# Optimization experiments

Measured on AMD Instinct MI355X. Metric: run time of the kernel, lower is better.

Reference implementation:

```python
import jax, jax.numpy as jnp
import numpy as np

B, M, FIN, K, FOUT, NNZ = 8, 40000, 64, 6, 64, 320000

def setup_inputs() -> dict:
    key = jax.random.key(0)
    k1, k2, k3, k4, k5 = jax.random.split(key, 5)
    x = jax.random.normal(k1, (B, M, FIN), dtype=jnp.float32)
    edge_rows = jax.random.randint(k2, (NNZ,), 0, M)
    edge_cols = jax.random.randint(k3, (NNZ,), 0, M)
    edge_vals = jax.random.normal(k4, (NNZ,), dtype=jnp.float32) * 0.1
    W = jax.random.normal(k5, (FIN * K, FOUT), dtype=jnp.float32) * 0.05
    return {"x": x, "edge_vals": edge_vals, "W": W,
            "edge_rows": edge_rows, "edge_cols": edge_cols}

def reference(x, edge_vals, W, edge_rows, edge_cols):
    Bd, Md, Fin = x.shape
    nK = W.shape[0] // Fin
    Fout = W.shape[1]
    # x0: [M, Fin*B] as in tf.transpose([1,2,0]) + reshape
    x0 = jnp.transpose(x, (1, 2, 0)).reshape(Md, Fin * Bd)

    def spmm_rescaled(v):
        # rescale_L(L, lmax=2) = L - I, so (L - I) @ v = L@v - v
        Lv = jax.ops.segment_sum(edge_vals[:, None] * v[edge_cols],
                                 edge_rows, num_segments=Md)
        return Lv - v

    xs = [x0]
    if nK > 1:
        x1 = spmm_rescaled(x0)
        xs.append(x1)
        xp, xc = x0, x1
        for _ in range(2, nK):
            xn = 2.0 * spmm_rescaled(xc) - xp  # Chebyshev recurrence
            xs.append(xn)
            xp, xc = xc, xn
    X = jnp.stack(xs, axis=0)                     # [K, M, Fin*B]
    X = X.reshape(nK, Md, Fin, Bd)                # split Fin*B -> (Fin, B)
    X = jnp.transpose(X, (3, 1, 2, 0))            # [B, M, Fin, K]
    X = X.reshape(Bd * Md, Fin * nK)
    out = (X @ W).reshape(Bd, Md, Fout)           # dense projection
    return out
```

## Files before the change

kernel.cpp:

```cpp
#include <hip/hip_runtime.h>

#define Mn    40000
#define Bn    8
#define FINn  64
#define Kn    6
#define FOUTn 64
#define NNZn  320000
#define Cn    512
#define NB    ((Mn + 255) / 256)
#define MT    (Mn / 64)


typedef _Float16 half8 __attribute__((ext_vector_type(8)));
typedef __attribute__((ext_vector_type(4))) float floatx4;

__device__ __forceinline__ ushort f2h(float f) {
    _Float16 h = (_Float16)f;
    return *(ushort*)&h;
}

__device__ __forceinline__ void gl_lds16(const ushort* g, ushort* l) {
    __builtin_amdgcn_global_load_lds(
        (const __attribute__((address_space(1))) unsigned int*)g,
        (__attribute__((address_space(3))) unsigned int*)l, 16, 0, 0);
}


__global__ __launch_bounds__(256) void k_hist(const int* __restrict__ rows,
                                              int* __restrict__ cnt) {
    int e = blockIdx.x * 256 + threadIdx.x;
    if (e < NNZn) atomicAdd(&cnt[rows[e]], 1);
}

__global__ __launch_bounds__(256) void k_scan_part(const int* __restrict__ cnt,
                                                   int* __restrict__ rowptr,
                                                   int* __restrict__ bsum) {
    __shared__ int part[256];
    int tid = threadIdx.x;
    int r = blockIdx.x * 256 + tid;
    int v = (r < Mn) ? cnt[r] : 0;
    part[tid] = v;
    __syncthreads();
    for (int off = 1; off < 256; off <<= 1) {
        int t = (tid >= off) ? part[tid - off] : 0;
        __syncthreads();
        part[tid] += t;
        __syncthreads();
    }
    if (r < Mn) rowptr[r] = part[tid] - v;
    if (tid == 255) bsum[blockIdx.x] = part[255];
}

__global__ __launch_bounds__(256) void k_scan_bsums(const int* __restrict__ bsum,
                                                    int* __restrict__ boff,
                                                    int* __restrict__ rowptr) {
    __shared__ int part[256];
    int tid = threadIdx.x;
    int v = (tid < NB) ? bsum[tid] : 0;
    part[tid] = v;
    __syncthreads();
    for (int off = 1; off < 256; off <<= 1) {
        int t = (tid >= off) ? part[tid - off] : 0;
        __syncthreads();
        part[tid] += t;
        __syncthreads();
    }
    if (tid < NB) boff[tid] = part[tid] - v;
    if (tid == 255) rowptr[Mn] = part[255];
}

__global__ __launch_bounds__(256) void k_scan_add(int* __restrict__ rowptr,
                                                  const int* __restrict__ boff,
                                                  int* __restrict__ wcur) {
    int r = blockIdx.x * 256 + threadIdx.x;
    if (r < Mn) {
        int v = rowptr[r] + boff[blockIdx.x];
        rowptr[r] = v;
        wcur[r] = v;
    }
}

__global__ __launch_bounds__(256) void k_scatter(const int* __restrict__ rows,
                                                 const int* __restrict__ cols,
                                                 const float* __restrict__ vals,
                                                 int* __restrict__ wcur,
                                                 int2* __restrict__ csr) {
    int e = blockIdx.x * 256 + threadIdx.x;
    if (e < NNZn) {
        int p = atomicAdd(&wcur[rows[e]], 1);
        int2 cv; cv.x = cols[e]; cv.y = __float_as_int(vals[e]);
        csr[p] = cv;
    }
}


__global__ __launch_bounds__(256) void k_transpose_h(const float* __restrict__ x,
                                                     ushort* __restrict__ x0h) {
    int m0 = blockIdx.x * 4;
    int t  = threadIdx.x;
#pragma unroll
    for (int k = 0; k < 2; ++k) {
        int i   = t + k * 256;
        int ml  = i >> 7;
        int rem = i & 127;
        int b   = rem >> 4;
        int fq  = (rem & 15) * 4;
        float4 a = *(const float4*)(x + ((size_t)b * Mn + m0 + ml) * 64 + fq);
        union { uint2 u; ushort h[4]; } s;
        s.h[0] = f2h(a.x); s.h[1] = f2h(a.y); s.h[2] = f2h(a.z); s.h[3] = f2h(a.w);
        *(uint2*)(x0h + (size_t)(m0 + ml) * Cn + b * 64 + fq) = s.u;
    }
}


__device__ __forceinline__ void fmah8(float* a, uint4 g, float w) {
    union { uint4 u; _Float16 h[8]; } c; c.u = g;
#pragma unroll
    for (int i = 0; i < 8; ++i) a[i] += w * (float)c.h[i];
}

__global__ __launch_bounds__(256) void k_spmm_h(const ushort* __restrict__ xc,
                                                const ushort* __restrict__ xp,
                                                ushort* __restrict__ xn,
                                                const int* __restrict__ rowptr,
                                                const int2* __restrict__ csr,
                                                int first) {
    int t = threadIdx.x;
    int lane = t & 63;
    int m = blockIdx.x * 4 + (t >> 6);
    const uint4* xc4 = (const uint4*)xc;
    uint4 v = xc4[(size_t)m * 64 + lane];
    uint4 p;
    if (!first) p = ((const uint4*)xp)[(size_t)m * 64 + lane];
    float a[8];
    { union { uint4 u; _Float16 h[8]; } c; c.u = v;
#pragma unroll
      for (int i = 0; i < 8; ++i) a[i] = -(float)c.h[i]; }

    int e = rowptr[m], end = rowptr[m + 1];
    for (; e + 8 <= end; e += 8) {
        int2 cv[8];
#pragma unroll
        for (int i = 0; i < 8; ++i) cv[i] = csr[e + i];
        uint4 g[8];
#pragma unroll
        for (int i = 0; i < 8; ++i) g[i] = xc4[(size_t)cv[i].x * 64 + lane];
#pragma unroll
        for (int i = 0; i < 8; ++i) fmah8(a, g[i], __int_as_float(cv[i].y));
    }
    for (; e + 4 <= end; e += 4) {
        int2 cv0 = csr[e],     cv1 = csr[e + 1];
        int2 cv2 = csr[e + 2], cv3 = csr[e + 3];
        uint4 g0 = xc4[(size_t)cv0.x * 64 + lane];
        uint4 g1 = xc4[(size_t)cv1.x * 64 + lane];
        uint4 g2 = xc4[(size_t)cv2.x * 64 + lane];
        uint4 g3 = xc4[(size_t)cv3.x * 64 + lane];
        fmah8(a, g0, __int_as_float(cv0.y));
        fmah8(a, g1, __int_as_float(cv1.y));
        fmah8(a, g2, __int_as_float(cv2.y));
        fmah8(a, g3, __int_as_float(cv3.y));
    }
    for (; e < end; ++e) {
        int2 cv = csr[e];
        uint4 g = xc4[(size_t)cv.x * 64 + lane];
        fmah8(a, g, __int_as_float(cv.y));
    }

    if (!first) {
        union { uint4 u; _Float16 h[8]; } c; c.u = p;
#pragma unroll
        for (int i = 0; i < 8; ++i) a[i] = 2.f * a[i] - (float)c.h[i];
    }
    union { uint4 u; _Float16 h[8]; } s;
#pragma unroll
    for (int i = 0; i < 8; ++i) s.h[i] = (_Float16)a[i];
    ((uint4*)xn)[(size_t)m * 64 + lane] = s.u;
}


__global__ __launch_bounds__(256) void k_wfrag(const float* __restrict__ W,
                                               ushort* __restrict__ wfrag) {
    int idx = blockIdx.x * 256 + threadIdx.x;
    if (idx >= 12 * 4 * 64 * 8) return;
    int j    = idx & 7;
    int lane = (idx >> 3) & 63;
    int n    = (idx >> 9) & 3;
    int kk   = idx >> 11;
    int k    = (lane >> 4) * 8 + j;
    int lev  = kk >> 1;
    int f    = (kk & 1) * 32 + k;
    int fo   = n * 16 + (lane & 15);
    wfrag[idx] = f2h(W[(f * Kn + lev) * FOUTn + fo]);
}


__global__ __launch_bounds__(256, 4) void k_gemm_mfma(const ushort* __restrict__ xh,
                                                      const ushort* __restrict__ wfrag,
                                                      float* __restrict__ out) {
    __shared__ __align__(16) ushort As[2][4096];
    int t     = threadIdx.x;
    int wv    = t >> 6;
    int lane  = t & 63;
    int q     = lane >> 4, r = lane & 15;
    int mtile = blockIdx.x % MT;
    int b     = blockIdx.x / MT;
    int m0    = mtile * 64;
    int swz   = r & 7;

    const size_t lstrideH = (size_t)Mn * Cn;

    const ushort* wfb = wfrag + ((size_t)wv * 64 + lane) * 8;
    half8 wf0  = *(const half8*)(wfb);
    half8 wf1  = *(const half8*)(wfb + 1 * 2048);
    half8 wf2  = *(const half8*)(wfb + 2 * 2048);
    half8 wf3  = *(const half8*)(wfb + 3 * 2048);
    half8 wf4  = *(const half8*)(wfb + 4 * 2048);
    half8 wf5  = *(const half8*)(wfb + 5 * 2048);
    half8 wf6  = *(const half8*)(wfb + 6 * 2048);
    half8 wf7  = *(const half8*)(wfb + 7 * 2048);
    half8 wf8  = *(const half8*)(wfb + 8 * 2048);
    half8 wf9  = *(const half8*)(wfb + 9 * 2048);
    half8 wf10 = *(const half8*)(wfb + 10 * 2048);
    half8 wf11 = *(const half8*)(wfb + 11 * 2048);

    int srow = wv * 8 + (lane >> 3);
    int gsw  = (lane & 7) ^ (srow & 7);
    const ushort* gsA = xh + (size_t)(m0 + srow) * Cn + b * 64 + gsw * 8;
    const ushort* gsB = gsA + 32 * (size_t)Cn;

    floatx4 acc0 = (floatx4)0.f, acc1 = (floatx4)0.f;
    floatx4 acc2 = (floatx4)0.f, acc3 = (floatx4)0.f;

#define STAGE(lev, buf) do {                                          \
        gl_lds16(gsA + (size_t)(lev) * lstrideH, &As[buf][wv * 512]); \
        gl_lds16(gsB + (size_t)(lev) * lstrideH, &As[buf][2048 + wv * 512]); \
    } while (0)

#define AF(buf, sub, half) \
    (*(const half8*)&As[buf][((sub) * 16 + r) * 64 + (((((half) * 4) + q) ^ swz) << 3)])

#define LEVEL(lev, buf, VMSTR, WFA, WFB) do {                                         \
        asm volatile("s_waitcnt vmcnt(" VMSTR ")" ::: "memory");                      \
        __syncthreads();                                                              \
        half8 a00 = AF(buf, 0, 0); half8 a10 = AF(buf, 1, 0);                         \
        half8 a20 = AF(buf, 2, 0); half8 a30 = AF(buf, 3, 0);                         \
        half8 a01 = AF(buf, 0, 1); half8 a11 = AF(buf, 1, 1);                         \
        half8 a21 = AF(buf, 2, 1); half8 a31 = AF(buf, 3, 1);                         \
        acc0 = __builtin_amdgcn_mfma_f32_16x16x32_f16(a00, WFA, acc0, 0, 0, 0);       \
        acc1 = __builtin_amdgcn_mfma_f32_16x16x32_f16(a10, WFA, acc1, 0, 0, 0);       \
        acc2 = __builtin_amdgcn_mfma_f32_16x16x32_f16(a20, WFA, acc2, 0, 0, 0);       \
        acc3 = __builtin_amdgcn_mfma_f32_16x16x32_f16(a30, WFA, acc3, 0, 0, 0);       \
        acc0 = __builtin_amdgcn_mfma_f32_16x16x32_f16(a01, WFB, acc0, 0, 0, 0);       \
        acc1 = __builtin_amdgcn_mfma_f32_16x16x32_f16(a11, WFB, acc1, 0, 0, 0);       \
        acc2 = __builtin_amdgcn_mfma_f32_16x16x32_f16(a21, WFB, acc2, 0, 0, 0);       \
        acc3 = __builtin_amdgcn_mfma_f32_16x16x32_f16(a31, WFB, acc3, 0, 0, 0);       \
        __syncthreads();                                                              \
        if ((lev) < 4) STAGE((lev) + 2, buf);                                         \
    } while (0)

    STAGE(0, 0);
    STAGE(1, 1);
    LEVEL(0, 0, "2", wf0,  wf1);
    LEVEL(1, 1, "2", wf2,  wf3);
    LEVEL(2, 0, "2", wf4,  wf5);
    LEVEL(3, 1, "2", wf6,  wf7);
    LEVEL(4, 0, "2", wf8,  wf9);
    LEVEL(5, 1, "0", wf10, wf11);

#undef LEVEL
#undef AF
#undef STAGE

#pragma unroll
    for (int sub = 0; sub < 4; ++sub) {
        floatx4 av = (sub == 0) ? acc0 : (sub == 1) ? acc1 : (sub == 2) ? acc2 : acc3;
#pragma unroll
        for (int reg = 0; reg < 4; ++reg) {
            size_t o = ((size_t)b * Mn + m0 + sub * 16 + q * 4 + reg) * FOUTn
                     + wv * 16 + r;
            out[o] = av[reg];
        }
    }
}


__global__ __launch_bounds__(512) void k_transpose_f(const float* __restrict__ x,
                                                     float* __restrict__ x0) {
    int m = blockIdx.x, t = threadIdx.x;
    int b = t >> 6, f = t & 63;
    x0[(size_t)m * Cn + t] = x[((size_t)b * Mn + m) * 64 + f];
}

__global__ __launch_bounds__(256) void k_spmm_f32(const float4* __restrict__ xc,
                                                  const float4* __restrict__ xp,
                                                  float4* __restrict__ xn,
                                                  const int* __restrict__ rowptr,
                                                  const int2* __restrict__ csr,
                                                  int first) {
    int t = threadIdx.x;
    int lane = t & 63;
    int m = blockIdx.x * 4 + (t >> 6);
    size_t rb = (size_t)m * 128;
    float4 v0 = xc[rb + lane];
    float4 v1 = xc[rb + 64 + lane];
    float4 a0 = make_float4(-v0.x, -v0.y, -v0.z, -v0.w);
    float4 a1 = make_float4(-v1.x, -v1.y, -v1.z, -v1.w);
    int e = rowptr[m], end = rowptr[m + 1];
    for (; e < end; ++e) {
        int2 cv = csr[e];
        float w = __int_as_float(cv.y);
        const float4* r = xc + (size_t)cv.x * 128;
        float4 g0 = r[lane], g1 = r[64 + lane];
        a0.x += w * g0.x; a0.y += w * g0.y; a0.z += w * g0.z; a0.w += w * g0.w;
        a1.x += w * g1.x; a1.y += w * g1.y; a1.z += w * g1.z; a1.w += w * g1.w;
    }
    if (!first) {
        float4 p0 = xp[rb + lane];
        float4 p1 = xp[rb + 64 + lane];
        a0.x = 2.f * a0.x - p0.x; a0.y = 2.f * a0.y - p0.y;
        a0.z = 2.f * a0.z - p0.z; a0.w = 2.f * a0.w - p0.w;
        a1.x = 2.f * a1.x - p1.x; a1.y = 2.f * a1.y - p1.y;
        a1.z = 2.f * a1.z - p1.z; a1.w = 2.f * a1.w - p1.w;
    }
    xn[rb + lane] = a0;
    xn[rb + 64 + lane] = a1;
}

__global__ __launch_bounds__(256) void k_gemm2(const float* __restrict__ xa,
                                               const float* __restrict__ xb,
                                               const float* __restrict__ W,
                                               float* __restrict__ out,
                                               int ka, int kb, int accum) {
    __shared__ __align__(16) float Wa[64 * 64];
    __shared__ __align__(16) float Wb[64 * 64];
    __shared__ __align__(16) float xsa[4 * Cn];
    __shared__ __align__(16) float xsb[4 * Cn];
    int t = threadIdx.x;
    size_t m0 = (size_t)blockIdx.x * 4;
    for (int i = t; i < 4096; i += 256) {
        int f = i >> 6, fo = i & 63;
        Wa[i] = W[(f * Kn + ka) * FOUTn + fo];
        Wb[i] = W[(f * Kn + kb) * FOUTn + fo];
    }
    for (int i = t; i < 4 * Cn; i += 256) {
        xsa[i] = xa[m0 * Cn + i];
        xsb[i] = xb[m0 * Cn + i];
    }
    __syncthreads();
    int fo  = (t & 15) * 4;
    int idx = t >> 4;
    int m   = idx & 3;
    int bq  = idx >> 2;
    float4 acc0 = make_float4(0.f, 0.f, 0.f, 0.f);
    float4 acc1 = make_float4(0.f, 0.f, 0.f, 0.f);
    for (int f = 0; f < 64; ++f) {
        float4 wa = *(const float4*)&Wa[f * 64 + fo];
        float a0 = xsa[m * Cn + bq * 64 + f];
        float a1 = xsa[m * Cn + (bq + 4) * 64 + f];
        acc0.x += a0 * wa.x; acc0.y += a0 * wa.y; acc0.z += a0 * wa.z; acc0.w += a0 * wa.w;
        acc1.x += a1 * wa.x; acc1.y += a1 * wa.y; acc1.z += a1 * wa.z; acc1.w += a1 * wa.w;
        float4 wb = *(const float4*)&Wb[f * 64 + fo];
        float b0 = xsb[m * Cn + bq * 64 + f];
        float b1 = xsb[m * Cn + (bq + 4) * 64 + f];
        acc0.x += b0 * wb.x; acc0.y += b0 * wb.y; acc0.z += b0 * wb.z; acc0.w += b0 * wb.w;
        acc1.x += b1 * wb.x; acc1.y += b1 * wb.y; acc1.z += b1 * wb.z; acc1.w += b1 * wb.w;
    }
    size_t o0 = (((size_t)bq * Mn) + (m0 + m)) * FOUTn + fo;
    size_t o1 = (((size_t)(bq + 4) * Mn) + (m0 + m)) * FOUTn + fo;
    float4* out4_0 = (float4*)&out[o0];
    float4* out4_1 = (float4*)&out[o1];
    if (accum) {
        float4 c0 = *out4_0, c1 = *out4_1;
        acc0.x += c0.x; acc0.y += c0.y; acc0.z += c0.z; acc0.w += c0.w;
        acc1.x += c1.x; acc1.y += c1.y; acc1.z += c1.z; acc1.w += c1.w;
    }
    *out4_0 = acc0;
    *out4_1 = acc1;
}


extern "C" void kernel_launch(void* const* d_in, const int* in_sizes, int n_in,
                              void* d_out, int out_size, void* d_ws, size_t ws_size,
                              hipStream_t stream) {
    const float* x         = (const float*)d_in[0];
    const float* edge_vals = (const float*)d_in[1];
    const float* W         = (const float*)d_in[2];
    const int*   edge_rows = (const int*)d_in[3];
    const int*   edge_cols = (const int*)d_in[4];
    float* out = (float*)d_out;

    char* ws = (char*)d_ws;
    const size_t bufB = (size_t)Mn * Cn * sizeof(float);
    const size_t bufH = (size_t)Mn * Cn * sizeof(ushort);
    const size_t wfB  = 12 * 4 * 64 * 8 * sizeof(ushort);
    const size_t csrB = (size_t)(Mn + 4 + Mn) * 4 + (size_t)NNZn * 8;

    const int spmm_grid = Mn / 4;
    const int gemm_grid = MT * 8;

    if (ws_size >= 6 * bufH + wfB + csrB) {
        ushort* xh  = (ushort*)ws;
        ushort* wfr = (ushort*)(ws + 6 * bufH);
        int*    rowptr = (int*)(ws + 6 * bufH + wfB);
        int*    fill   = rowptr + (Mn + 4);
        int2*   csr    = (int2*)(fill + Mn);
        int*    bsum   = (int*)csr;
        int*    boff   = bsum + 256;
        ushort* slot[6];
        for (int l = 0; l < 6; ++l) slot[l] = xh + (size_t)l * Mn * Cn;

        hipMemsetAsync(fill, 0, Mn * sizeof(int), stream);
        k_hist<<<(NNZn + 255) / 256, 256, 0, stream>>>(edge_rows, fill);
        k_scan_part<<<NB, 256, 0, stream>>>(fill, rowptr, bsum);
        k_scan_bsums<<<1, 256, 0, stream>>>(bsum, boff, rowptr);
        k_scan_add<<<NB, 256, 0, stream>>>(rowptr, boff, fill);
        k_scatter<<<(NNZn + 255) / 256, 256, 0, stream>>>(edge_rows, edge_cols,
                                                          edge_vals, fill, csr);
        k_wfrag<<<96, 256, 0, stream>>>(W, wfr);

        k_transpose_h<<<Mn / 4, 256, 0, stream>>>(x, slot[0]);
        k_spmm_h<<<spmm_grid, 256, 0, stream>>>(slot[0], slot[0], slot[1],
                                                rowptr, csr, 1);
        k_spmm_h<<<spmm_grid, 256, 0, stream>>>(slot[1], slot[0], slot[2],
                                                rowptr, csr, 0);
        k_spmm_h<<<spmm_grid, 256, 0, stream>>>(slot[2], slot[1], slot[3],
                                                rowptr, csr, 0);
        k_spmm_h<<<spmm_grid, 256, 0, stream>>>(slot[3], slot[2], slot[4],
                                                rowptr, csr, 0);
        k_spmm_h<<<spmm_grid, 256, 0, stream>>>(slot[4], slot[3], slot[5],
                                                rowptr, csr, 0);
        k_gemm_mfma<<<gemm_grid, 256, 0, stream>>>(xh, wfr, out);
    } else {
        float* buf0 = (float*)(ws);
        float* buf1 = (float*)(ws + bufB);
        float* buf2 = (float*)(ws + 2 * bufB);
        int*   rowptr = (int*)(ws + 3 * bufB);
        int*   fill   = rowptr + (Mn + 4);
        int2*  csr    = (int2*)(fill + Mn);
        int*   bsum   = (int*)csr;
        int*   boff   = bsum + 256;
        hipMemsetAsync(fill, 0, Mn * sizeof(int), stream);
        k_hist<<<(NNZn + 255) / 256, 256, 0, stream>>>(edge_rows, fill);
        k_scan_part<<<NB, 256, 0, stream>>>(fill, rowptr, bsum);
        k_scan_bsums<<<1, 256, 0, stream>>>(bsum, boff, rowptr);
        k_scan_add<<<NB, 256, 0, stream>>>(rowptr, boff, fill);
        k_scatter<<<(NNZn + 255) / 256, 256, 0, stream>>>(edge_rows, edge_cols,
                                                          edge_vals, fill, csr);
        k_transpose_f<<<Mn, 512, 0, stream>>>(x, buf0);
        k_spmm_f32<<<Mn / 4, 256, 0, stream>>>((const float4*)buf0, (const float4*)buf0,
                                               (float4*)buf1, rowptr, csr, 1);
        k_gemm2<<<Mn / 4, 256, 0, stream>>>(buf0, buf1, W, out, 0, 1, 0);
        k_spmm_f32<<<Mn / 4, 256, 0, stream>>>((const float4*)buf1, (const float4*)buf0,
                                               (float4*)buf2, rowptr, csr, 0);
        k_spmm_f32<<<Mn / 4, 256, 0, stream>>>((const float4*)buf2, (const float4*)buf1,
                                               (float4*)buf0, rowptr, csr, 0);
        k_gemm2<<<Mn / 4, 256, 0, stream>>>(buf2, buf0, W, out, 2, 3, 1);
        k_spmm_f32<<<Mn / 4, 256, 0, stream>>>((const float4*)buf0, (const float4*)buf2,
                                               (float4*)buf1, rowptr, csr, 0);
        k_spmm_f32<<<Mn / 4, 256, 0, stream>>>((const float4*)buf1, (const float4*)buf0,
                                               (float4*)buf2, rowptr, csr, 0);
        k_gemm2<<<Mn / 4, 256, 0, stream>>>(buf1, buf2, W, out, 4, 5, 1);
    }
}
```

Baseline: 521.6 us.

## Split SpMM rows across edges and column chunks with shuffle reduction

The SpMM kernel now gives each wavefront one row and one 64-column chunk out of eight. The 8 edge-slots × 8 column lanes process different edges in parallel, then the partial sums are combined with xor-shuffles. This is meant to expose more memory-level parallelism for rows with few nonzeros (about 8 on average) instead of walking edges serially. In exchange the grid grows eightfold, rowptr, csr and self loads are repeated per column block, and the shuffle reduction adds overhead.

```diff
diff --git a/kernel.cpp b/kernel.cpp
--- a/kernel.cpp
+++ b/kernel.cpp
@@ -9,6 +9,8 @@
 #define Cn    512
 #define NB    ((Mn + 255) / 256)
 #define MT    (Mn / 64)
+#define NCB   8
+#define MCH   (Mn / 4)
 
 
 typedef _Float16 half8 __attribute__((ext_vector_type(8)));
@@ -125,56 +127,68 @@
                                                 const int* __restrict__ rowptr,
                                                 const int2* __restrict__ csr,
                                                 int first) {
-    int t = threadIdx.x;
+    int t    = threadIdx.x;
     int lane = t & 63;
-    int m = blockIdx.x * 4 + (t >> 6);
+    int wv   = t >> 6;
+    int es   = lane >> 3;
+    int cl   = lane & 7;
+    int cb   = blockIdx.x / MCH;
+    int mch  = blockIdx.x % MCH;
+    int m    = mch * 4 + wv;
+    int coff = cb * 8 + cl;
+
     const uint4* xc4 = (const uint4*)xc;
-    uint4 v = xc4[(size_t)m * 64 + lane];
+    uint4 v = xc4[(size_t)m * 64 + coff];
     uint4 p;
-    if (!first) p = ((const uint4*)xp)[(size_t)m * 64 + lane];
+    if (!first) p = ((const uint4*)xp)[(size_t)m * 64 + coff];
+    int rp0 = rowptr[m], rp1 = rowptr[m + 1];
+
     float a[8];
-    { union { uint4 u; _Float16 h[8]; } c; c.u = v;
-#pragma unroll
-      for (int i = 0; i < 8; ++i) a[i] = -(float)c.h[i]; }
-
-    int e = rowptr[m], end = rowptr[m + 1];
-    for (; e + 8 <= end; e += 8) {
-        int2 cv[8];
-#pragma unroll
-        for (int i = 0; i < 8; ++i) cv[i] = csr[e + i];
-        uint4 g[8];
-#pragma unroll
-        for (int i = 0; i < 8; ++i) g[i] = xc4[(size_t)cv[i].x * 64 + lane];
-#pragma unroll
-        for (int i = 0; i < 8; ++i) fmah8(a, g[i], __int_as_float(cv[i].y));
-    }
-    for (; e + 4 <= end; e += 4) {
-        int2 cv0 = csr[e],     cv1 = csr[e + 1];
-        int2 cv2 = csr[e + 2], cv3 = csr[e + 3];
-        uint4 g0 = xc4[(size_t)cv0.x * 64 + lane];
-        uint4 g1 = xc4[(size_t)cv1.x * 64 + lane];
-        uint4 g2 = xc4[(size_t)cv2.x * 64 + lane];
-        uint4 g3 = xc4[(size_t)cv3.x * 64 + lane];
+#pragma unroll
+    for (int i = 0; i < 8; ++i) a[i] = 0.f;
+
+    int e = rp0;
+    for (; e + 16 <= rp1; e += 16) {
+        int2 cv0 = csr[e + es];
+        int2 cv1 = csr[e + 8 + es];
+        uint4 g0 = xc4[(size_t)cv0.x * 64 + coff];
+        uint4 g1 = xc4[(size_t)cv1.x * 64 + coff];
         fmah8(a, g0, __int_as_float(cv0.y));
         fmah8(a, g1, __int_as_float(cv1.y));
-        fmah8(a, g2, __int_as_float(cv2.y));
-        fmah8(a, g3, __int_as_float(cv3.y));
-    }
-    for (; e < end; ++e) {
-        int2 cv = csr[e];
-        uint4 g = xc4[(size_t)cv.x * 64 + lane];
+    }
+    for (; e + 8 <= rp1; e += 8) {
+        int2 cv = csr[e + es];
+        uint4 g = xc4[(size_t)cv.x * 64 + coff];
         fmah8(a, g, __int_as_float(cv.y));
     }
-
+    if (e < rp1) {
+        int idx = e + es;
+        bool ok = idx < rp1;
+        int2 cv = csr[ok ? idx : rp0];
+        uint4 g = xc4[(size_t)cv.x * 64 + coff];
+        fmah8(a, g, ok ? __int_as_float(cv.y) : 0.f);
+    }
+
+#pragma unroll
+    for (int s = 8; s < 64; s <<= 1) {
+#pragma unroll
+        for (int i = 0; i < 8; ++i) a[i] += __shfl_xor(a[i], s, 64);
+    }
+
+    { union { uint4 u; _Float16 h[8]; } c; c.u = v;
+#pragma unroll
+      for (int i = 0; i < 8; ++i) a[i] -= (float)c.h[i]; }
     if (!first) {
         union { uint4 u; _Float16 h[8]; } c; c.u = p;
 #pragma unroll
         for (int i = 0; i < 8; ++i) a[i] = 2.f * a[i] - (float)c.h[i];
     }
-    union { uint4 u; _Float16 h[8]; } s;
-#pragma unroll
-    for (int i = 0; i < 8; ++i) s.h[i] = (_Float16)a[i];
-    ((uint4*)xn)[(size_t)m * 64 + lane] = s.u;
+    if (es == 0) {
+        union { uint4 u; _Float16 h[8]; } s;
+#pragma unroll
+        for (int i = 0; i < 8; ++i) s.h[i] = (_Float16)a[i];
+        ((uint4*)xn)[(size_t)m * 64 + coff] = s.u;
+    }
 }
 
 
@@ -395,7 +409,7 @@
     const size_t wfB  = 12 * 4 * 64 * 8 * sizeof(ushort);
     const size_t csrB = (size_t)(Mn + 4 + Mn) * 4 + (size_t)NNZn * 8;
 
-    const int spmm_grid = Mn / 4;
+    const int spmm_grid = NCB * MCH;
     const int gemm_grid = MT * 8;
 
     if (ws_size >= 6 * bufH + wfB + csrB) {
```

New measurement: 738.1 us. +41.5%, slower.
